# Kernel optimization log

Measured on AMD Instinct MI355X. Metric: run time of the kernel, lower is better.

Reference implementation:

```python
import jax, jax.numpy as jnp
from jax import lax
import numpy as np

# int24 / PrecisionSplit constants (all exactly representable in float32)
TWO12 = 4096.0      # 2**12
TWO13 = 8192.0      # 2**13
TWO23 = 8388608.0   # 2**23
TWO24 = 16777216.0  # 2**24
TWO25 = 33554432.0  # 2**25

N_ITER = 64
N_CHANNELS = 256
BATCH = 4096


def _wrap(v, half, full):
    # two's-complement wrap of integer-valued floats to signed range [-half, half)
    return jnp.mod(v + half, full) - half


def _cast_up_i24(v):
    # GMACv2(int24, [1]) on a single input: round to integer grid and wrap to int24
    return _wrap(jnp.round(v), TWO23, TWO24)


def setup_inputs() -> dict:
    key = jax.random.key(0)
    k1, _ = jax.random.split(key)
    # scale so values exercise a wide chunk of the int24 range after rounding
    x = jax.random.normal(k1, (BATCH, N_ITER * N_CHANNELS), dtype=jnp.float32) * 1.0e5
    s_init = jnp.zeros((N_CHANNELS,), dtype=jnp.float32)
    return {"x": x, "s_init": s_init}


def reference(x, s_init):
    B = x.shape[0]
    n_ch = s_init.shape[0]
    n_iter = x.shape[-1] // n_ch

    # cast_up1 / cast_up2: quantize inputs to int24
    x_i = _cast_up_i24(x)            # [B, n_iter*n_ch]
    s0 = _cast_up_i24(s_init)        # [n_ch]
    s0 = jnp.broadcast_to(s0, (B, n_ch))

    # i24SumLoop: sequential GMAC accumulate with int24 wrapping per step.
    # Per-step partial sums stay within |v| < 2**24 so float32 stays exact.
    xs = x_i.reshape(B, n_iter, n_ch).transpose(1, 0, 2)  # [n_iter, B, n_ch]

    def step(carry, xi):
        s = _wrap(carry + xi, TWO23, TWO24)
        return s, None

    y, _ = lax.scan(step, s0, xs)    # [B, n_ch], int24-wrapped

    # PrecisionSplit([12, 13], [16, 16]): split (up to 25-bit) value into
    # low 12 bits (unsigned) and high 13 bits (signed), each held in 16-bit words.
    y_u = jnp.mod(y, TWO25)                             # unsigned 25-bit view
    y_lo = jnp.mod(y_u, TWO12)                          # low 12 bits
    y_hi = _wrap(jnp.floor(y_u / TWO12), TWO12, TWO13)  # high 13 bits, signed
    return (y_lo, y_hi)
```

## Files before the change

### kernel.cpp

```cpp
#include <hip/hip_runtime.h>
#include <cstdint>

#define N_ITER 64
#define N_CH 256
#define BATCH 4096
#define OUT_PLANE (BATCH * N_CH)

__device__ __forceinline__ void split_ref_fp32(int y, float& lo, float& hi) {
    uint32_t u;
    if (y >= 0) {
        u = (uint32_t)y;
    } else {
        u = (uint32_t)(y + 33554432);
        int m = y & 3;
        if (m == 1)      u -= 1u;
        else if (m == 3) u += 1u;
    }
    lo = (float)(u & 0xFFFu);
    int q = (int)(u >> 12);
    hi = (float)(((q + 4096) & 8191) - 4096);
}

__global__ __launch_bounds__(256) void i24sum_kernel(const float* __restrict__ x,
                                                     const float* __restrict__ s_init,
                                                     float* __restrict__ out) {
    const int tid  = threadIdx.x;
    const int lane = tid & 63;
    const int row  = blockIdx.x * 4 + (tid >> 6);

    const float4* xr = reinterpret_cast<const float4*>(x) + (size_t)row * (N_ITER * N_CH / 4);
    const float4  s4 = reinterpret_cast<const float4*>(s_init)[lane];

    int ax = (int)rintf(s4.x);
    int ay = (int)rintf(s4.y);
    int az = (int)rintf(s4.z);
    int aw = (int)rintf(s4.w);

#pragma unroll 16
    for (int i = 0; i < N_ITER; ++i) {
        float4 v = xr[i * (N_CH / 4) + lane];
        ax += (int)rintf(v.x);
        ay += (int)rintf(v.y);
        az += (int)rintf(v.z);
        aw += (int)rintf(v.w);
    }

    ax = (ax << 8) >> 8;
    ay = (ay << 8) >> 8;
    az = (az << 8) >> 8;
    aw = (aw << 8) >> 8;

    float4 lo4, hi4;
    split_ref_fp32(ax, lo4.x, hi4.x);
    split_ref_fp32(ay, lo4.y, hi4.y);
    split_ref_fp32(az, lo4.z, hi4.z);
    split_ref_fp32(aw, lo4.w, hi4.w);

    const int ovec = (row * N_CH) / 4 + lane;
    reinterpret_cast<float4*>(out)[ovec] = lo4;
    reinterpret_cast<float4*>(out + OUT_PLANE)[ovec] = hi4;
}

extern "C" void kernel_launch(void* const* d_in, const int* in_sizes, int n_in,
                              void* d_out, int out_size, void* d_ws, size_t ws_size,
                              hipStream_t stream) {
    const float* x      = (const float*)d_in[0];
    const float* s_init = (const float*)d_in[1];
    float*       out    = (float*)d_out;

    dim3 grid(BATCH / 4);
    dim3 block(256);
    i24sum_kernel<<<grid, block, 0, stream>>>(x, s_init, out);
}
```

Baseline: 359.5 us.

## Split each row's iteration sum across four waves with LDS reduction

Each block now handles one batch row instead of four, with each of its four waves summing a quarter of the 64 iterations before a shared-memory reduction finishes the total. Input loads become nontemporal. The aim is more independent loads in flight per row and a larger grid to hide memory latency on a streaming, bandwidth-bound kernel. The cost is a block-level barrier, an LDS round trip, and only one wave doing the split and store.

```diff
diff --git a/kernel.cpp b/kernel.cpp
--- a/kernel.cpp
+++ b/kernel.cpp
@@ -6,7 +6,11 @@
 #define BATCH 4096
 #define OUT_PLANE (BATCH * N_CH)
 
-__device__ __forceinline__ void split_ref_fp32(int y, float& lo, float& hi) {
+typedef float v4f __attribute__((ext_vector_type(4)));
+typedef int   v4i __attribute__((ext_vector_type(4)));
+typedef float v2f __attribute__((ext_vector_type(2)));
+
+__device__ __forceinline__ v2f split_ref_fp32(int y) {
     uint32_t u;
     if (y >= 0) {
         u = (uint32_t)y;
@@ -16,9 +20,11 @@
         if (m == 1)      u -= 1u;
         else if (m == 3) u += 1u;
     }
-    lo = (float)(u & 0xFFFu);
+    v2f r;
+    r.x = (float)(u & 0xFFFu);
     int q = (int)(u >> 12);
-    hi = (float)(((q + 4096) & 8191) - 4096);
+    r.y = (float)(((q + 4096) & 8191) - 4096);
+    return r;
 }
 
 __global__ __launch_bounds__(256) void i24sum_kernel(const float* __restrict__ x,
@@ -26,39 +32,57 @@
                                                      float* __restrict__ out) {
     const int tid  = threadIdx.x;
     const int lane = tid & 63;
-    const int row  = blockIdx.x * 4 + (tid >> 6);
+    const int wave = tid >> 6;
+    const int row  = blockIdx.x;
 
-    const float4* xr = reinterpret_cast<const float4*>(x) + (size_t)row * (N_ITER * N_CH / 4);
-    const float4  s4 = reinterpret_cast<const float4*>(s_init)[lane];
+    const v4f* xr = reinterpret_cast<const v4f*>(x) + (size_t)row * (N_ITER * N_CH / 4);
 
-    int ax = (int)rintf(s4.x);
-    int ay = (int)rintf(s4.y);
-    int az = (int)rintf(s4.z);
-    int aw = (int)rintf(s4.w);
-
-#pragma unroll 16
-    for (int i = 0; i < N_ITER; ++i) {
-        float4 v = xr[i * (N_CH / 4) + lane];
-        ax += (int)rintf(v.x);
-        ay += (int)rintf(v.y);
-        az += (int)rintf(v.z);
-        aw += (int)rintf(v.w);
+    v4i acc = (v4i)0;
+#pragma unroll
+    for (int k = 0; k < 16; ++k) {
+        const int i = (wave << 4) + k;
+        v4f v = __builtin_nontemporal_load(xr + i * (N_CH / 4) + lane);
+        acc.x += (int)rintf(v.x);
+        acc.y += (int)rintf(v.y);
+        acc.z += (int)rintf(v.z);
+        acc.w += (int)rintf(v.w);
     }
 
-    ax = (ax << 8) >> 8;
-    ay = (ay << 8) >> 8;
-    az = (az << 8) >> 8;
-    aw = (aw << 8) >> 8;
+    __shared__ v4i part[4][64];
+    part[wave][lane] = acc;
+    __syncthreads();
 
-    float4 lo4, hi4;
-    split_ref_fp32(ax, lo4.x, hi4.x);
-    split_ref_fp32(ay, lo4.y, hi4.y);
-    split_ref_fp32(az, lo4.z, hi4.z);
-    split_ref_fp32(aw, lo4.w, hi4.w);
+    if (wave == 0) {
+        const v4f s4 = reinterpret_cast<const v4f*>(s_init)[lane];
+        v4i t = part[0][lane];
+        t += part[1][lane];
+        t += part[2][lane];
+        t += part[3][lane];
+        t.x += (int)rintf(s4.x);
+        t.y += (int)rintf(s4.y);
+        t.z += (int)rintf(s4.z);
+        t.w += (int)rintf(s4.w);
 
-    const int ovec = (row * N_CH) / 4 + lane;
-    reinterpret_cast<float4*>(out)[ovec] = lo4;
-    reinterpret_cast<float4*>(out + OUT_PLANE)[ovec] = hi4;
+        t.x = (t.x << 8) >> 8;
+        t.y = (t.y << 8) >> 8;
+        t.z = (t.z << 8) >> 8;
+        t.w = (t.w << 8) >> 8;
+
+        const v2f sx = split_ref_fp32(t.x);
+        const v2f sy = split_ref_fp32(t.y);
+        const v2f sz = split_ref_fp32(t.z);
+        const v2f sw = split_ref_fp32(t.w);
+
+        v4f lo4, hi4;
+        lo4.x = sx.x; hi4.x = sx.y;
+        lo4.y = sy.x; hi4.y = sy.y;
+        lo4.z = sz.x; hi4.z = sz.y;
+        lo4.w = sw.x; hi4.w = sw.y;
+
+        const int ovec = row * (N_CH / 4) + lane;
+        reinterpret_cast<v4f*>(out)[ovec] = lo4;
+        reinterpret_cast<v4f*>(out + OUT_PLANE)[ovec] = hi4;
+    }
 }
 
 extern "C" void kernel_launch(void* const* d_in, const int* in_sizes, int n_in,
@@ -68,7 +92,7 @@
     const float* s_init = (const float*)d_in[1];
     float*       out    = (float*)d_out;
 
-    dim3 grid(BATCH / 4);
+    dim3 grid(BATCH);
     dim3 block(256);
     i24sum_kernel<<<grid, block, 0, stream>>>(x, s_init, out);
 }
```

Result: faster. 335.3 us (-6.7%).
